# Kernel optimization log

Hardware: AMD Instinct MI355X
Metric: run time of the kernel (lower is better)

Reference implementation:

```python
import jax, jax.numpy as jnp
import numpy as np

EPS = 1e-8  # torch.nn.CosineSimilarity default eps
V, I, H, L = 50257, 1024, 1024, 16384  # vocab, gru_input_size, gru_hidden_size, max_length


def setup_inputs() -> dict:
    key = jax.random.key(0)
    ks = jax.random.split(key, 12)
    rn = lambda k, shape, s=1.0: jax.random.normal(k, shape, dtype=jnp.float32) * s
    return {
        "token": jax.random.randint(ks[0], (1, 1), 0, V),
        "hidden": rn(ks[1], (1, 1, H)),
        "encoder_outputs": rn(ks[2], (L, H)),
        "emb": rn(ks[3], (V, I)),
        "attn_w": rn(ks[4], (H, I + H), 0.02), "attn_b": jnp.zeros((H,), jnp.float32),
        "comb_w": rn(ks[5], (I, I + H), 0.02), "comb_b": jnp.zeros((I,), jnp.float32),
        "w_ih": rn(ks[6], (3 * H, I), 0.02), "w_hh": rn(ks[7], (3 * H, H), 0.02),
        "b_ih": jnp.zeros((3 * H,), jnp.float32), "b_hh": jnp.zeros((3 * H,), jnp.float32),
        "fc2_w": rn(ks[8], (64, H), 0.02), "fc2_b": jnp.zeros((64,), jnp.float32),
        "out_w": rn(ks[9], (1, 64), 0.02), "out_b": jnp.zeros((1,), jnp.float32),
    }


def reference(token, hidden, encoder_outputs, emb, attn_w, attn_b, comb_w, comb_b,
              w_ih, w_hh, b_ih, b_hh, fc2_w, fc2_b, out_w, out_b):
    # 'identifier'/'keyword' branch; dropout is identity in eval mode.
    embedded = emb[token[0, 0]][None, :]                      # [1, I]
    h0 = hidden[0]                                            # [1, H]
    # attention query projection
    q = jnp.concatenate([embedded, h0], axis=1) @ attn_w.T + attn_b  # [1, H]
    # cosine similarity of q vs each encoder output row (dim=1 broadcast)
    qn = jnp.maximum(jnp.linalg.norm(q[0]), EPS)
    en = jnp.maximum(jnp.linalg.norm(encoder_outputs, axis=1), EPS)  # [L]
    sims = (encoder_outputs @ q[0]) / (qn * en)               # [L]
    attn_weights = jax.nn.softmax(sims)[None, :]              # [1, L]
    attn_applied = attn_weights @ encoder_outputs             # [1, H]
    x = jnp.concatenate([embedded, attn_applied], axis=1) @ comb_w.T + comb_b  # [1, I]
    x = jax.nn.relu(x)
    # single GRU cell step (PyTorch gate convention: r, z, n)
    gi = x @ w_ih.T + b_ih                                    # [1, 3H]
    gh = h0 @ w_hh.T + b_hh                                   # [1, 3H]
    r = jax.nn.sigmoid(gi[:, :H] + gh[:, :H])
    z = jax.nn.sigmoid(gi[:, H:2 * H] + gh[:, H:2 * H])
    n = jnp.tanh(gi[:, 2 * H:] + r * gh[:, 2 * H:])
    h_new = (1.0 - z) * n + z * h0                            # [1, H]
    out = jax.nn.relu(h_new @ fc2_w.T + fc2_b) @ out_w.T + out_b  # [1, 1]
    return out, h_new[None], attn_weights
```

## Files before the change

kernel.cpp:

```cpp
#include <hip/hip_runtime.h>
#include <hip/hip_bf16.h>
#include <math.h>

#define II 1024
#define HH 1024
#define LL 16384
#define EPSF 1e-8f
#define XBLK 64
#define SC_AA 4294967296.0f
#define ISC_AA 2.3283064365386963e-10f
#define SC_DEN 1.099511627776e12f
#define ISC_DEN 9.094947017729282e-13f
#define SC_GI 4294967296.0f
#define ISC_GI 2.3283064365386963e-10f

typedef unsigned long long ull;

__device__ __forceinline__ float wred_sum(float v) {
    #pragma unroll
    for (int o = 32; o; o >>= 1) v += __shfl_down(v, o);
    return v;
}

__global__ __launch_bounds__(256) void n1_kernel(
    const int* __restrict__ token, const float* __restrict__ emb,
    const float* __restrict__ hidden, const float* __restrict__ attn_w,
    const float* __restrict__ attn_b, const float* __restrict__ w_hh,
    const float* __restrict__ b_hh, const float* __restrict__ comb_w,
    const float* __restrict__ comb_b, float* __restrict__ q,
    float* __restrict__ gh, float* __restrict__ x_emb,
    ull* __restrict__ accs) {
    if (blockIdx.x == 0) {
        for (int i = threadIdx.x; i < 1024 + 1 + 3072 + 1; i += 256)
            accs[i] = 0ull;
    }
    int w = (blockIdx.x * blockDim.x + threadIdx.x) >> 6;
    int lane = threadIdx.x & 63;
    const float* er = emb + (size_t)token[0] * II;
    if (w < HH) {
        const float* row = attn_w + (size_t)w * (II + HH);
        float acc = 0.f;
        for (int k = lane * 4; k < II + HH; k += 256) {
            float4 w4 = *(const float4*)(row + k);
            const float* src = (k < II) ? (er + k) : (hidden + (k - II));
            float4 x4 = *(const float4*)src;
            acc += w4.x * x4.x + w4.y * x4.y + w4.z * x4.z + w4.w * x4.w;
        }
        acc = wred_sum(acc);
        if (lane == 0) q[w] = acc + attn_b[w];
    } else if (w < 4 * HH) {
        int r = w - HH;
        const float* row = w_hh + (size_t)r * HH;
        float acc = 0.f;
        for (int k = lane * 4; k < HH; k += 256) {
            float4 w4 = *(const float4*)(row + k);
            float4 x4 = *(const float4*)(hidden + k);
            acc += w4.x * x4.x + w4.y * x4.y + w4.z * x4.z + w4.w * x4.w;
        }
        acc = wred_sum(acc);
        if (lane == 0) gh[r] = acc + b_hh[r];
    } else {
        int r = w - 4 * HH;
        const float* row = comb_w + (size_t)r * (II + HH);
        float acc = 0.f;
        #pragma unroll
        for (int k = lane * 4; k < II; k += 256) {
            float4 w4 = *(const float4*)(row + k);
            float4 x4 = *(const float4*)(er + k);
            acc += w4.x * x4.x + w4.y * x4.y + w4.z * x4.z + w4.w * x4.w;
        }
        acc = wred_sum(acc);
        if (lane == 0) x_emb[r] = acc + comb_b[r];
    }
}

__global__ __launch_bounds__(1024) void n2_kernel(
    const float* __restrict__ enc, const float* __restrict__ q,
    float* __restrict__ e_out, ull* __restrict__ aa_int,
    ull* __restrict__ den_int) {
    __shared__ float s_w[64];
    const int b = blockIdx.x, t = threadIdx.x;
    const int wv = t >> 6, lane = t & 63;

    float4 q4[4];
    #pragma unroll
    for (int j = 0; j < 4; ++j) q4[j] = *(const float4*)(q + lane * 4 + j * 256);
    float ss = 0.f;
    #pragma unroll
    for (int j = 0; j < 4; ++j)
        ss += q4[j].x * q4[j].x + q4[j].y * q4[j].y + q4[j].z * q4[j].z +
              q4[j].w * q4[j].w;
    ss = wred_sum(ss);
    ss = __shfl(ss, 0);
    const float qn = fmaxf(sqrtf(ss), EPSF);

    #pragma unroll
    for (int j = 0; j < 4; ++j) {
        int r = b * 64 + wv * 4 + j;
        const float* row = enc + (size_t)r * HH;
        float dv = 0.f, sv = 0.f;
        #pragma unroll
        for (int k = 0; k < 4; ++k) {
            float4 e4 = *(const float4*)(row + lane * 4 + k * 256);
            dv += e4.x * q4[k].x + e4.y * q4[k].y + e4.z * q4[k].z +
                  e4.w * q4[k].w;
            sv += e4.x * e4.x + e4.y * e4.y + e4.z * e4.z + e4.w * e4.w;
        }
        #pragma unroll
        for (int o = 32; o; o >>= 1) {
            dv += __shfl_down(dv, o);
            sv += __shfl_down(sv, o);
        }
        if (lane == 0) {
            float en = fmaxf(sqrtf(sv), EPSF);
            float e = expf(dv / (qn * en) - 1.f);
            s_w[wv * 4 + j] = e;
            e_out[r] = e;
        }
    }
    __syncthreads();

    if (wv == 0) {
        float v = s_w[lane];
        v = wred_sum(v);
        if (lane == 0)
            atomicAdd(den_int, (ull)(long long)llrintf(v * SC_DEN));
    }
    const float* base = enc + (size_t)b * 64 * HH;
    float acc = 0.f;
    #pragma unroll 8
    for (int r = 0; r < 64; ++r)
        acc = fmaf(s_w[r], base[(size_t)r * HH + t], acc);
    atomicAdd(&aa_int[t], (ull)(long long)llrintf(acc * SC_AA));
}

__global__ __launch_bounds__(1024) void n3_kernel(
    const float* __restrict__ comb_w, const float* __restrict__ x_emb,
    const float* __restrict__ w_ih, const float* __restrict__ b_ih,
    const float* __restrict__ gh, const float* __restrict__ hidden,
    const float* __restrict__ fc2_w, const float* __restrict__ fc2_b,
    const float* __restrict__ out_w, const float* __restrict__ out_b,
    const float* __restrict__ e_in, const ull* __restrict__ aa_int,
    const ull* __restrict__ den_int, ull* __restrict__ gi_acc,
    ull* __restrict__ gc, float* __restrict__ h_new,
    float* __restrict__ out_scalar, float* __restrict__ attn_wout) {
    __shared__ float s_aa[HH];
    __shared__ float s_x[16];
    __shared__ float hsh[HH];
    __shared__ float f[64];
    __shared__ unsigned s_last;
    const int b = blockIdx.x, t = threadIdx.x;
    const int wv = t >> 6, lane = t & 63;

    const float inv_den = 1.f / ((float)((long long)den_int[0]) * ISC_DEN);
    s_aa[t] = (float)((long long)aa_int[t]) * ISC_AA * inv_den;
    if (t < 256) {
        int i = b * 256 + t;
        attn_wout[i] = e_in[i] * inv_den;
    }
    __syncthreads();

    int r = b * 16 + wv;
    {
        const float* row = comb_w + (size_t)r * (II + HH) + II;
        float acc = 0.f;
        #pragma unroll
        for (int k = lane * 4; k < HH; k += 256) {
            float4 w4 = *(const float4*)(row + k);
            acc += w4.x * s_aa[k] + w4.y * s_aa[k + 1] + w4.z * s_aa[k + 2] +
                   w4.w * s_aa[k + 3];
        }
        acc = wred_sum(acc);
        if (lane == 0) s_x[wv] = fmaxf(acc + x_emb[r], 0.f);
    }
    __syncthreads();

    const int c0 = b * 16;
    #pragma unroll
    for (int i = 0; i < 3; ++i) {
        int rr = t + i * 1024;
        const float* wrow = w_ih + (size_t)rr * II + c0;
        float4 w0 = *(const float4*)(wrow + 0);
        float4 w1 = *(const float4*)(wrow + 4);
        float4 w2 = *(const float4*)(wrow + 8);
        float4 w3 = *(const float4*)(wrow + 12);
        float acc = w0.x * s_x[0] + w0.y * s_x[1] + w0.z * s_x[2] +
                    w0.w * s_x[3] + w1.x * s_x[4] + w1.y * s_x[5] +
                    w1.z * s_x[6] + w1.w * s_x[7] + w2.x * s_x[8] +
                    w2.y * s_x[9] + w2.z * s_x[10] + w2.w * s_x[11] +
                    w3.x * s_x[12] + w3.y * s_x[13] + w3.z * s_x[14] +
                    w3.w * s_x[15];
        atomicAdd(&gi_acc[rr], (ull)(long long)llrintf(acc * SC_GI));
    }
    __syncthreads();
    if (t == 0) {
        __threadfence();
        ull old = atomicAdd(gc, 1ull);
        s_last = (old + 1ull == (ull)XBLK) ? 1u : 0u;
    }
    __syncthreads();
    if (!s_last) return;
    __threadfence();

    float gr = (float)((long long)gi_acc[t]) * ISC_GI + b_ih[t];
    float gz = (float)((long long)gi_acc[HH + t]) * ISC_GI + b_ih[HH + t];
    float gn = (float)((long long)gi_acc[2 * HH + t]) * ISC_GI + b_ih[2 * HH + t];
    float rg = 1.f / (1.f + expf(-(gr + gh[t])));
    float zg = 1.f / (1.f + expf(-(gz + gh[HH + t])));
    float ng = tanhf(gn + rg * gh[2 * HH + t]);
    float h = (1.f - zg) * ng + zg * hidden[t];
    hsh[t] = h;
    h_new[t] = h;
    __syncthreads();
    #pragma unroll
    for (int rr = 0; rr < 4; ++rr) {
        int r2 = wv * 4 + rr;
        const float* row = fc2_w + (size_t)r2 * HH;
        float acc = 0.f;
        #pragma unroll
        for (int k = lane * 4; k < HH; k += 256) {
            float4 w4 = *(const float4*)(row + k);
            acc += w4.x * hsh[k] + w4.y * hsh[k + 1] + w4.z * hsh[k + 2] +
                   w4.w * hsh[k + 3];
        }
        acc = wred_sum(acc);
        if (lane == 0) f[r2] = fmaxf(acc + fc2_b[r2], 0.f);
    }
    __syncthreads();
    if (t < 64) {
        float v = f[t] * out_w[t];
        v = wred_sum(v);
        if (t == 0) out_scalar[0] = v + out_b[0];
    }
}

extern "C" void kernel_launch(void* const* d_in, const int* in_sizes, int n_in,
                              void* d_out, int out_size, void* d_ws,
                              size_t ws_size, hipStream_t stream) {
    const int*   token  = (const int*)d_in[0];
    const float* hidden = (const float*)d_in[1];
    const float* enc    = (const float*)d_in[2];
    const float* emb    = (const float*)d_in[3];
    const float* attn_w = (const float*)d_in[4];
    const float* attn_b = (const float*)d_in[5];
    const float* comb_w = (const float*)d_in[6];
    const float* comb_b = (const float*)d_in[7];
    const float* w_ih   = (const float*)d_in[8];
    const float* w_hh   = (const float*)d_in[9];
    const float* b_ih   = (const float*)d_in[10];
    const float* b_hh   = (const float*)d_in[11];
    const float* fc2_w  = (const float*)d_in[12];
    const float* fc2_b  = (const float*)d_in[13];
    const float* out_w  = (const float*)d_in[14];
    const float* out_b  = (const float*)d_in[15];

    float* ws = (float*)d_ws;
    float* q     = ws;
    float* gh    = ws + 1024;
    float* x_emb = ws + 4096;
    float* e     = ws + 5120;
    ull* accs    = (ull*)(ws + 21504);
    ull* aa_int  = accs;
    ull* den_int = accs + 1024;
    ull* gi_acc  = accs + 1025;
    ull* gc      = accs + 4097;

    float* out_scalar = (float*)d_out;
    float* h_new      = (float*)d_out + 1;
    float* attn_wout  = (float*)d_out + 1 + HH;

    n1_kernel<<<1280, 256, 0, stream>>>(token, emb, hidden, attn_w, attn_b,
                                        w_hh, b_hh, comb_w, comb_b, q, gh,
                                        x_emb, accs);
    n2_kernel<<<256, 1024, 0, stream>>>(enc, q, e, aa_int, den_int);
    n3_kernel<<<XBLK, 1024, 0, stream>>>(comb_w, x_emb, w_ih, b_ih, gh, hidden,
                                         fc2_w, fc2_b, out_w, out_b, e, aa_int,
                                         den_int, gi_acc, gc, h_new, out_scalar,
                                         attn_wout);
}
```

Measured before the change: 63.64 us.

## Move GRU hidden and comb-emb GEMVs into attention kernel, replicate atomic accumulators

Shrinks the first kernel to just the query projection, so the critical path before the attention pass is shorter. The w_hh and comb_w-embedding GEMVs now run inside the attention kernel, which also computes the weighted sum of encoder rows from registers instead of re-reading the encoder rows. The softmax denominator becomes per-block partial sums in float instead of a global integer atomic. The aa and gi accumulators are split into 4 and 2 replicas to reduce atomic contention. n3 also prefetches fc2_w to warm the cache. The trade-off is more registers and 64KB of shared memory in n2, and a float-order-dependent denominator.

New measurement: 56.38 us (median of 2 runs). 11.4% less time.

```diff
diff --git a/kernel.cpp b/kernel.cpp
--- a/kernel.cpp
+++ b/kernel.cpp
@@ -9,8 +9,6 @@
 #define XBLK 64
 #define SC_AA 4294967296.0f
 #define ISC_AA 2.3283064365386963e-10f
-#define SC_DEN 1.099511627776e12f
-#define ISC_DEN 9.094947017729282e-13f
 #define SC_GI 4294967296.0f
 #define ISC_GI 2.3283064365386963e-10f
 
@@ -19,39 +17,115 @@
 __device__ __forceinline__ float wred_sum(float v) {
     #pragma unroll
     for (int o = 32; o; o >>= 1) v += __shfl_down(v, o);
+    return v;
+}
+__device__ __forceinline__ float wred_sum_all(float v) {
+    #pragma unroll
+    for (int o = 32; o; o >>= 1) v += __shfl_xor(v, o);
     return v;
 }
 
 __global__ __launch_bounds__(256) void n1_kernel(
     const int* __restrict__ token, const float* __restrict__ emb,
     const float* __restrict__ hidden, const float* __restrict__ attn_w,
-    const float* __restrict__ attn_b, const float* __restrict__ w_hh,
-    const float* __restrict__ b_hh, const float* __restrict__ comb_w,
-    const float* __restrict__ comb_b, float* __restrict__ q,
-    float* __restrict__ gh, float* __restrict__ x_emb,
+    const float* __restrict__ attn_b, float* __restrict__ q,
     ull* __restrict__ accs) {
-    if (blockIdx.x == 0) {
-        for (int i = threadIdx.x; i < 1024 + 1 + 3072 + 1; i += 256)
-            accs[i] = 0ull;
-    }
+    for (int i = blockIdx.x * 256 + threadIdx.x; i < 10241; i += 65536)
+        accs[i] = 0ull;
     int w = (blockIdx.x * blockDim.x + threadIdx.x) >> 6;
     int lane = threadIdx.x & 63;
     const float* er = emb + (size_t)token[0] * II;
-    if (w < HH) {
-        const float* row = attn_w + (size_t)w * (II + HH);
-        float acc = 0.f;
-        for (int k = lane * 4; k < II + HH; k += 256) {
-            float4 w4 = *(const float4*)(row + k);
-            const float* src = (k < II) ? (er + k) : (hidden + (k - II));
-            float4 x4 = *(const float4*)src;
-            acc += w4.x * x4.x + w4.y * x4.y + w4.z * x4.z + w4.w * x4.w;
-        }
-        acc = wred_sum(acc);
-        if (lane == 0) q[w] = acc + attn_b[w];
-    } else if (w < 4 * HH) {
-        int r = w - HH;
+    const float* row = attn_w + (size_t)w * (II + HH);
+    float acc = 0.f;
+    for (int k = lane * 4; k < II + HH; k += 256) {
+        float4 w4 = *(const float4*)(row + k);
+        const float* src = (k < II) ? (er + k) : (hidden + (k - II));
+        float4 x4 = *(const float4*)src;
+        acc += w4.x * x4.x + w4.y * x4.y + w4.z * x4.z + w4.w * x4.w;
+    }
+    acc = wred_sum(acc);
+    if (lane == 0) q[w] = acc + attn_b[w];
+}
+
+__global__ __launch_bounds__(1024) void n2_kernel(
+    const int* __restrict__ token, const float* __restrict__ emb,
+    const float* __restrict__ enc, const float* __restrict__ q,
+    const float* __restrict__ hidden, const float* __restrict__ w_hh,
+    const float* __restrict__ b_hh, const float* __restrict__ comb_w,
+    const float* __restrict__ comb_b, float* __restrict__ e_out,
+    float* __restrict__ psum, float* __restrict__ gh,
+    float* __restrict__ x_emb, ull* __restrict__ aa_int) {
+    __shared__ float s_colw[16][1024];
+    __shared__ float s_red[16];
+    const int b = blockIdx.x, t = threadIdx.x;
+    const int wv = t >> 6, lane = t & 63;
+
+    float4 q4[4];
+    #pragma unroll
+    for (int j = 0; j < 4; ++j) q4[j] = *(const float4*)(q + lane * 4 + j * 256);
+    float ss = 0.f;
+    #pragma unroll
+    for (int j = 0; j < 4; ++j)
+        ss += q4[j].x * q4[j].x + q4[j].y * q4[j].y + q4[j].z * q4[j].z +
+              q4[j].w * q4[j].w;
+    ss = wred_sum_all(ss);
+    const float qn = fmaxf(sqrtf(ss), EPSF);
+
+    float cs[16];
+    #pragma unroll
+    for (int i = 0; i < 16; ++i) cs[i] = 0.f;
+    float ewave = 0.f;
+    #pragma unroll
+    for (int j = 0; j < 4; ++j) {
+        int r = b * 64 + wv * 4 + j;
+        const float* row = enc + (size_t)r * HH;
+        float4 e4[4];
+        float dv = 0.f, sv = 0.f;
+        #pragma unroll
+        for (int k = 0; k < 4; ++k) {
+            e4[k] = *(const float4*)(row + lane * 4 + k * 256);
+            dv += e4[k].x * q4[k].x + e4[k].y * q4[k].y + e4[k].z * q4[k].z +
+                  e4[k].w * q4[k].w;
+            sv += e4[k].x * e4[k].x + e4[k].y * e4[k].y + e4[k].z * e4[k].z +
+                  e4[k].w * e4[k].w;
+        }
+        dv = wred_sum_all(dv);
+        sv = wred_sum_all(sv);
+        float en = fmaxf(sqrtf(sv), EPSF);
+        float e = expf(dv / (qn * en) - 1.f);
+        if (lane == 0) e_out[r] = e;
+        ewave += e;
+        #pragma unroll
+        for (int k = 0; k < 4; ++k) {
+            cs[k * 4 + 0] = fmaf(e, e4[k].x, cs[k * 4 + 0]);
+            cs[k * 4 + 1] = fmaf(e, e4[k].y, cs[k * 4 + 1]);
+            cs[k * 4 + 2] = fmaf(e, e4[k].z, cs[k * 4 + 2]);
+            cs[k * 4 + 3] = fmaf(e, e4[k].w, cs[k * 4 + 3]);
+        }
+    }
+    #pragma unroll
+    for (int k = 0; k < 4; ++k)
+        *(float4*)&s_colw[wv][k * 256 + lane * 4] = *(float4*)&cs[k * 4];
+    if (lane == 0) s_red[wv] = ewave;
+    __syncthreads();
+    if (wv == 0) {
+        float v = (lane < 16) ? s_red[lane] : 0.f;
+        v = wred_sum(v);
+        if (lane == 0) psum[b] = v;
+    }
+    {
+        float a = 0.f;
+        #pragma unroll
+        for (int w = 0; w < 16; ++w) a += s_colw[w][t];
+        atomicAdd(&aa_int[(b & 3) * 1024 + t],
+                  (ull)(long long)llrintf(a * SC_AA));
+    }
+
+    if (wv < 12) {
+        int r = b * 12 + wv;
         const float* row = w_hh + (size_t)r * HH;
         float acc = 0.f;
+        #pragma unroll
         for (int k = lane * 4; k < HH; k += 256) {
             float4 w4 = *(const float4*)(row + k);
             float4 x4 = *(const float4*)(hidden + k);
@@ -60,8 +134,9 @@
         acc = wred_sum(acc);
         if (lane == 0) gh[r] = acc + b_hh[r];
     } else {
-        int r = w - 4 * HH;
+        int r = b * 4 + (wv - 12);
         const float* row = comb_w + (size_t)r * (II + HH);
+        const float* er = emb + (size_t)token[0] * II;
         float acc = 0.f;
         #pragma unroll
         for (int k = lane * 4; k < II; k += 256) {
@@ -72,66 +147,6 @@
         acc = wred_sum(acc);
         if (lane == 0) x_emb[r] = acc + comb_b[r];
     }
-}
-
-__global__ __launch_bounds__(1024) void n2_kernel(
-    const float* __restrict__ enc, const float* __restrict__ q,
-    float* __restrict__ e_out, ull* __restrict__ aa_int,
-    ull* __restrict__ den_int) {
-    __shared__ float s_w[64];
-    const int b = blockIdx.x, t = threadIdx.x;
-    const int wv = t >> 6, lane = t & 63;
-
-    float4 q4[4];
-    #pragma unroll
-    for (int j = 0; j < 4; ++j) q4[j] = *(const float4*)(q + lane * 4 + j * 256);
-    float ss = 0.f;
-    #pragma unroll
-    for (int j = 0; j < 4; ++j)
-        ss += q4[j].x * q4[j].x + q4[j].y * q4[j].y + q4[j].z * q4[j].z +
-              q4[j].w * q4[j].w;
-    ss = wred_sum(ss);
-    ss = __shfl(ss, 0);
-    const float qn = fmaxf(sqrtf(ss), EPSF);
-
-    #pragma unroll
-    for (int j = 0; j < 4; ++j) {
-        int r = b * 64 + wv * 4 + j;
-        const float* row = enc + (size_t)r * HH;
-        float dv = 0.f, sv = 0.f;
-        #pragma unroll
-        for (int k = 0; k < 4; ++k) {
-            float4 e4 = *(const float4*)(row + lane * 4 + k * 256);
-            dv += e4.x * q4[k].x + e4.y * q4[k].y + e4.z * q4[k].z +
-                  e4.w * q4[k].w;
-            sv += e4.x * e4.x + e4.y * e4.y + e4.z * e4.z + e4.w * e4.w;
-        }
-        #pragma unroll
-        for (int o = 32; o; o >>= 1) {
-            dv += __shfl_down(dv, o);
-            sv += __shfl_down(sv, o);
-        }
-        if (lane == 0) {
-            float en = fmaxf(sqrtf(sv), EPSF);
-            float e = expf(dv / (qn * en) - 1.f);
-            s_w[wv * 4 + j] = e;
-            e_out[r] = e;
-        }
-    }
-    __syncthreads();
-
-    if (wv == 0) {
-        float v = s_w[lane];
-        v = wred_sum(v);
-        if (lane == 0)
-            atomicAdd(den_int, (ull)(long long)llrintf(v * SC_DEN));
-    }
-    const float* base = enc + (size_t)b * 64 * HH;
-    float acc = 0.f;
-    #pragma unroll 8
-    for (int r = 0; r < 64; ++r)
-        acc = fmaf(s_w[r], base[(size_t)r * HH + t], acc);
-    atomicAdd(&aa_int[t], (ull)(long long)llrintf(acc * SC_AA));
 }
 
 __global__ __launch_bounds__(1024) void n3_kernel(
@@ -140,8 +155,8 @@
     const float* __restrict__ gh, const float* __restrict__ hidden,
     const float* __restrict__ fc2_w, const float* __restrict__ fc2_b,
     const float* __restrict__ out_w, const float* __restrict__ out_b,
-    const float* __restrict__ e_in, const ull* __restrict__ aa_int,
-    const ull* __restrict__ den_int, ull* __restrict__ gi_acc,
+    const float* __restrict__ e_in, const float* __restrict__ psum,
+    const ull* __restrict__ aa_int, ull* __restrict__ gi_acc,
     ull* __restrict__ gc, float* __restrict__ h_new,
     float* __restrict__ out_scalar, float* __restrict__ attn_wout) {
     __shared__ float s_aa[HH];
@@ -152,11 +167,25 @@
     const int b = blockIdx.x, t = threadIdx.x;
     const int wv = t >> 6, lane = t & 63;
 
-    const float inv_den = 1.f / ((float)((long long)den_int[0]) * ISC_DEN);
-    s_aa[t] = (float)((long long)aa_int[t]) * ISC_AA * inv_den;
+    float4 p4 = *(const float4*)(psum + lane * 4);
+    float den = wred_sum_all(p4.x + p4.y + p4.z + p4.w);
+    const float inv_den = 1.f / den;
+
+    s_aa[t] = (float)((long long)(aa_int[t] + aa_int[1024 + t] +
+                                  aa_int[2048 + t] + aa_int[3072 + t])) *
+              ISC_AA * inv_den;
     if (t < 256) {
         int i = b * 256 + t;
         attn_wout[i] = e_in[i] * inv_den;
+    }
+    {
+        float sw = 0.f;
+        #pragma unroll
+        for (int i = 0; i < 16; ++i) {
+            float4 v = *(const float4*)(fc2_w + t * 4 + i * 4096);
+            sw += v.x + v.y + v.z + v.w;
+        }
+        asm volatile("" :: "v"(sw));
     }
     __syncthreads();
 
@@ -176,6 +205,7 @@
     __syncthreads();
 
     const int c0 = b * 16;
+    ull* grep = gi_acc + (size_t)(b & 1) * 3072;
     #pragma unroll
     for (int i = 0; i < 3; ++i) {
         int rr = t + i * 1024;
@@ -190,7 +220,7 @@
                     w2.y * s_x[9] + w2.z * s_x[10] + w2.w * s_x[11] +
                     w3.x * s_x[12] + w3.y * s_x[13] + w3.z * s_x[14] +
                     w3.w * s_x[15];
-        atomicAdd(&gi_acc[rr], (ull)(long long)llrintf(acc * SC_GI));
+        atomicAdd(&grep[rr], (ull)(long long)llrintf(acc * SC_GI));
     }
     __syncthreads();
     if (t == 0) {
@@ -202,9 +232,13 @@
     if (!s_last) return;
     __threadfence();
 
-    float gr = (float)((long long)gi_acc[t]) * ISC_GI + b_ih[t];
-    float gz = (float)((long long)gi_acc[HH + t]) * ISC_GI + b_ih[HH + t];
-    float gn = (float)((long long)gi_acc[2 * HH + t]) * ISC_GI + b_ih[2 * HH + t];
+    float gr = (float)((long long)(gi_acc[t] + gi_acc[3072 + t])) * ISC_GI +
+               b_ih[t];
+    float gz = (float)((long long)(gi_acc[HH + t] + gi_acc[3072 + HH + t])) *
+                   ISC_GI + b_ih[HH + t];
+    float gn = (float)((long long)(gi_acc[2 * HH + t] +
+                                   gi_acc[3072 + 2 * HH + t])) * ISC_GI +
+               b_ih[2 * HH + t];
     float rg = 1.f / (1.f + expf(-(gr + gh[t])));
     float zg = 1.f / (1.f + expf(-(gz + gh[HH + t])));
     float ng = tanhf(gn + rg * gh[2 * HH + t]);
@@ -213,8 +247,8 @@
     h_new[t] = h;
     __syncthreads();
     #pragma unroll
-    for (int rr = 0; rr < 4; ++rr) {
-        int r2 = wv * 4 + rr;
+    for (int rr2 = 0; rr2 < 4; ++rr2) {
+        int r2 = wv * 4 + rr2;
         const float* row = fc2_w + (size_t)r2 * HH;
         float acc = 0.f;
         #pragma unroll
@@ -259,22 +293,23 @@
     float* gh    = ws + 1024;
     float* x_emb = ws + 4096;
     float* e     = ws + 5120;
-    ull* accs    = (ull*)(ws + 21504);
+    float* psum  = ws + 21504;
+    ull* accs    = (ull*)(ws + 21760);
     ull* aa_int  = accs;
-    ull* den_int = accs + 1024;
-    ull* gi_acc  = accs + 1025;
-    ull* gc      = accs + 4097;
+    ull* gi_acc  = accs + 4096;
+    ull* gc      = accs + 10240;
 
     float* out_scalar = (float*)d_out;
     float* h_new      = (float*)d_out + 1;
     float* attn_wout  = (float*)d_out + 1 + HH;
 
-    n1_kernel<<<1280, 256, 0, stream>>>(token, emb, hidden, attn_w, attn_b,
-                                        w_hh, b_hh, comb_w, comb_b, q, gh,
-                                        x_emb, accs);
-    n2_kernel<<<256, 1024, 0, stream>>>(enc, q, e, aa_int, den_int);
+    n1_kernel<<<256, 256, 0, stream>>>(token, emb, hidden, attn_w, attn_b, q,
+                                       accs);
+    n2_kernel<<<256, 1024, 0, stream>>>(token, emb, enc, q, hidden, w_hh, b_hh,
+                                        comb_w, comb_b, e, psum, gh, x_emb,
+                                        aa_int);
     n3_kernel<<<XBLK, 1024, 0, stream>>>(comb_w, x_emb, w_ih, b_ih, gh, hidden,
-                                         fc2_w, fc2_b, out_w, out_b, e, aa_int,
-                                         den_int, gi_acc, gc, h_new, out_scalar,
+                                         fc2_w, fc2_b, out_w, out_b, e, psum,
+                                         aa_int, gi_acc, gc, h_new, out_scalar,
                                          attn_wout);
 }
```
